# Optimization experiments

Measured on AMD Instinct MI355X. Metric: run time of the kernel, lower is better.

The kernel has to match this reference:

```python
import jax, jax.numpy as jnp
import numpy as np

B, S, D = 4, 2048, 1024  # batch, seq_len, input_dimension
KD, VD = 1024, 1024      # key_dim, value_dim


def setup_inputs() -> dict:
    key = jax.random.key(0)
    ks = jax.random.split(key, 9)
    sc_in = 1.0 / np.sqrt(D)
    sc_v = 1.0 / np.sqrt(VD)
    return {
        "x":  jax.random.normal(ks[0], (B, S, D), dtype=jnp.float32),
        "Wq": jax.random.normal(ks[1], (KD, D), dtype=jnp.float32) * sc_in,
        "bq": jax.random.normal(ks[2], (KD,), dtype=jnp.float32) * 0.01,
        "Wk": jax.random.normal(ks[3], (KD, D), dtype=jnp.float32) * sc_in,
        "bk": jax.random.normal(ks[4], (KD,), dtype=jnp.float32) * 0.01,
        "Wv": jax.random.normal(ks[5], (VD, D), dtype=jnp.float32) * sc_in,
        "bv": jax.random.normal(ks[6], (VD,), dtype=jnp.float32) * 0.01,
        "Wo": jax.random.normal(ks[7], (D, VD), dtype=jnp.float32) * sc_v,
        "bo": jax.random.normal(ks[8], (D,), dtype=jnp.float32) * 0.01,
    }


def reference(x, Wq, bq, Wk, bk, Wv, bv, Wo, bo):
    # projections (torch Linear: x @ W.T + b)
    q = jnp.einsum('bsd,kd->bsk', x, Wq) + bq   # (B,S,KD)
    k = jnp.einsum('bsd,kd->bsk', x, Wk) + bk   # (B,S,KD)
    v = jnp.einsum('bsd,vd->bsv', x, Wv) + bv   # (B,S,VD)

    scores = jnp.einsum('bqk,bsk->bqs', q, k) / jnp.sqrt(jnp.float32(KD))  # (B,S,S)

    # sign rescale: scores * sign(scores) (sign(0) mapped to 1) == |scores| with zeros kept
    sign_mask = jnp.sign(scores)
    sign_mask = sign_mask + (sign_mask == 0).astype(jnp.float32)

    # causal mask: lower-triangular (incl diag) multiplied by 1, strict upper -> -inf
    seq = scores.shape[-1]
    causal = jnp.tril(jnp.ones((seq, seq), dtype=bool))
    masked = jnp.where(causal, scores * sign_mask, -jnp.inf)

    weights = jax.nn.softmax(masked, axis=2)            # (B,S,S)
    out = jnp.einsum('bqs,bsv->bqv', weights, v)        # (B,S,VD)
    return jnp.einsum('bqv,dv->bqd', out, Wo) + bo      # (B,S,D)
```

## Files before the change

### kernel.cpp

```cpp
#include <hip/hip_runtime.h>
#include <hip/hip_bf16.h>
#include <cstdint>


#define BM 128

typedef __attribute__((ext_vector_type(8))) __bf16 bf16x8;
typedef __attribute__((ext_vector_type(4))) __bf16 bf16x4;
typedef __attribute__((ext_vector_type(4))) float floatx4;

struct Ptr3 { const float* p[3]; };

__device__ __forceinline__ void async_copy16(const __bf16* g, const __bf16* l) {
  __builtin_amdgcn_global_load_lds(
      (const __attribute__((address_space(1))) unsigned int*)(const void*)g,
      (__attribute__((address_space(3))) unsigned int*)(unsigned)(uintptr_t)(const void*)l,
      16, 0, 0);
}

__device__ __forceinline__ void gemm_core(const __bf16* __restrict__ pA,
                                          const __bf16* __restrict__ pB,
                                          int K, int kBeg, int kEnd, int mb,
                                          int nb, floatx4 (&acc)[4][4]) {
  __shared__ __align__(16) __bf16 As0[BM * 32];
  __shared__ __align__(16) __bf16 As1[BM * 32];
  __shared__ __align__(16) __bf16 Bs0[BM * 32];
  __shared__ __align__(16) __bf16 Bs1[BM * 32];

  const int t = threadIdx.x;
  const int lane = t & 63;
  const int wave = t >> 6;
  const int quad = lane >> 4;
  const int l16 = lane & 15;
  const int wm = wave >> 1;
  const int wn = wave & 1;

  const __bf16* gA = pA + (long)(mb * BM + (t >> 2)) * K + ((t & 3) * 8);
  const __bf16* gB = pB + (long)(nb * BM + (t >> 2)) * K + ((t & 3) * 8);
  const long rowHalf = (long)64 * K;
  __bf16* lA0 = &As0[t * 8];
  __bf16* lA1 = &As1[t * 8];
  __bf16* lB0 = &Bs0[t * 8];
  __bf16* lB1 = &Bs1[t * 8];

  for (int kk = kBeg; kk < kEnd; ++kk) {
    const long ko = (long)kk * 64;
    async_copy16(gA + ko, lA0);
    async_copy16(gA + ko + rowHalf, lA0 + 2048);
    async_copy16(gA + ko + 32, lA1);
    async_copy16(gA + ko + 32 + rowHalf, lA1 + 2048);
    async_copy16(gB + ko, lB0);
    async_copy16(gB + ko + rowHalf, lB0 + 2048);
    async_copy16(gB + ko + 32, lB1);
    async_copy16(gB + ko + 32 + rowHalf, lB1 + 2048);
    __syncthreads();

#pragma unroll
    for (int p = 0; p < 2; ++p) {
      const __bf16* As = p ? As1 : As0;
      const __bf16* Bs = p ? Bs1 : Bs0;
      bf16x8 af[4], bfr[4];
#pragma unroll
      for (int i = 0; i < 4; ++i) {
        af[i] = *(const bf16x8*)&As[(wm * 64 + i * 16 + l16) * 32 + quad * 8];
        bfr[i] = *(const bf16x8*)&Bs[(wn * 64 + i * 16 + l16) * 32 + quad * 8];
      }
#pragma unroll
      for (int i = 0; i < 4; ++i)
#pragma unroll
        for (int j = 0; j < 4; ++j)
          acc[i][j] = __builtin_amdgcn_mfma_f32_16x16x32_bf16(af[i], bfr[j],
                                                              acc[i][j], 0, 0, 0);
    }
    __syncthreads();
  }
}

__global__ void prep2(const float* __restrict__ Wo, Ptr3 tp,
                      const float* __restrict__ bv, const float* __restrict__ bq,
                      const float* __restrict__ bk,
                      __bf16* __restrict__ Wob, __bf16* __restrict__ Wqt,
                      __bf16* __restrict__ Wkt, __bf16* __restrict__ Wvt,
                      float* __restrict__ bvo, float* __restrict__ cscal,
                      float* __restrict__ lsum) {
  __shared__ __bf16 tile[64][66];
  __shared__ float wsum[4];
  const int bid = blockIdx.x;
  const int t = threadIdx.x;
  if (bid < 1024) {
    const long e = ((long)bid * 256 + t) * 4;
    const float4 f = *(const float4*)(Wo + e);
    bf16x4 o;
    o[0] = (__bf16)f.x; o[1] = (__bf16)f.y; o[2] = (__bf16)f.z; o[3] = (__bf16)f.w;
    *(bf16x4*)(Wob + e) = o;
  } else if (bid < 1792) {
    const int seg = (bid - 1024) >> 8;
    const int idx = (bid - 1024) & 255;
    const float* src = tp.p[seg];
    __bf16* dstw = seg == 0 ? Wqt : (seg == 1 ? Wkt : Wvt);
    const int r0 = (idx >> 4) * 64, c0 = (idx & 15) * 64;
#pragma unroll
    for (int e = 0; e < 16; ++e) {
      const int i = e * 256 + t;
      const int r = i >> 6, c = i & 63;
      tile[r][c] = (__bf16)src[(long)(r0 + r) * 1024 + (c0 + c)];
    }
    __syncthreads();
#pragma unroll
    for (int e = 0; e < 16; ++e) {
      const int i = e * 256 + t;
      const int r = i >> 6, c = i & 63;
      dstw[(long)(c0 + r) * 1024 + (r0 + c)] = tile[c][r];
    }
  } else if (bid < 2816) {
    const int d = bid - 1792;
    const float* row = Wo + (long)d * 1024;
    float s = 0.f;
    for (int v = t; v < 1024; v += 256) s += bv[v] * row[v];
#pragma unroll
    for (int off = 32; off > 0; off >>= 1) s += __shfl_down(s, off, 64);
    if ((t & 63) == 0) wsum[t >> 6] = s;
    __syncthreads();
    if (t == 0) bvo[d] = wsum[0] + wsum[1] + wsum[2] + wsum[3];
  } else if (bid == 2816) {
    float s = 0.f;
    for (int i = t; i < 1024; i += 256) s += bq[i] * bk[i];
#pragma unroll
    for (int off = 32; off > 0; off >>= 1) s += __shfl_down(s, off, 64);
    if ((t & 63) == 0) wsum[t >> 6] = s;
    __syncthreads();
    if (t == 0) *cscal = wsum[0] + wsum[1] + wsum[2] + wsum[3];
  } else {
#pragma unroll
    for (int e = 0; e < 8; ++e)
      *(float4*)(lsum + (e * 256 + t) * 4) = float4{0.f, 0.f, 0.f, 0.f};
  }
}

__global__ void __launch_bounds__(256, 3)
gemmA(const __bf16* __restrict__ Wkt, const __bf16* __restrict__ Wqt,
      const __bf16* __restrict__ Wob, const __bf16* __restrict__ Wvt,
      __bf16* __restrict__ Mt, __bf16* __restrict__ Wvo,
      const float* __restrict__ bk, const float* __restrict__ bq,
      float* __restrict__ m1f, float* __restrict__ m2f,
      const float* __restrict__ x, __bf16* __restrict__ xb) {
  const int id = blockIdx.x;
  const int t = threadIdx.x;

  if (id >= 160) {
    const long i = ((long)(id - 160) * 256 + t) * 4;
    const float4 f = *(const float4*)(x + i);
    bf16x4 o;
    o[0] = (__bf16)f.x; o[1] = (__bf16)f.y; o[2] = (__bf16)f.z; o[3] = (__bf16)f.w;
    *(bf16x4*)(xb + i) = o;
    return;
  }
  if (id >= 128) {
    const int q = (id - 128) & 15;
    const bool isM2 = (id - 128) >= 16;
    const __bf16* Wt = isM2 ? Wkt : Wqt;
    const float* bvec = isM2 ? bq : bk;
    float* dst = isM2 ? m2f : m1f;
    const int lane = t & 63, wave = t >> 6, qd = lane >> 4, l16 = lane & 15;
#pragma unroll
    for (int rr = 0; rr < 4; ++rr) {
      const int row = q * 64 + (wave * 4 + qd) * 4 + rr;
      const __bf16* wr = Wt + (long)row * 1024 + l16 * 64;
      const float* bp = bvec + l16 * 64;
      float s = 0.f;
#pragma unroll
      for (int jj = 0; jj < 8; ++jj) {
        bf16x8 wv = *(const bf16x8*)(wr + jj * 8);
#pragma unroll
        for (int e = 0; e < 8; ++e) s += (float)wv[e] * bp[jj * 8 + e];
      }
      s += __shfl_xor(s, 1, 64);
      s += __shfl_xor(s, 2, 64);
      s += __shfl_xor(s, 4, 64);
      s += __shfl_xor(s, 8, 64);
      if (l16 == 0) dst[row] = s;
    }
    return;
  }

  const __bf16 *pA, *pB;
  __bf16* dst;
  int mb, nb;
  if (id < 64) {
    mb = id >> 3; nb = id & 7;
    pA = Wkt; pB = Wqt; dst = Mt;
  } else {
    const int w = id - 64;
    mb = w >> 3; nb = w & 7;
    pA = Wob; pB = Wvt; dst = Wvo;
  }

  floatx4 acc[4][4] = {};
  gemm_core(pA, pB, 1024, 0, 16, mb, nb, acc);

  const int lane = t & 63, wave = t >> 6;
  const int rb = (wave >> 1) * 64 + (lane >> 4) * 4;
  const int cb = (wave & 1) * 64 + (lane & 15);
#pragma unroll
  for (int j4 = 0; j4 < 4; ++j4) {
    const int gc = nb * 128 + cb + j4 * 16;
#pragma unroll
    for (int i = 0; i < 4; ++i) {
      const int gr = mb * BM + rb + i * 16;
#pragma unroll
      for (int r = 0; r < 4; ++r)
        dst[(long)(gr + r) * 1024 + gc] = (__bf16)acc[i][j4][r];
    }
  }
}

__global__ void __launch_bounds__(256, 3)
gemmB1(const __bf16* __restrict__ xb, const __bf16* __restrict__ Mt,
       const float* __restrict__ m2f, __bf16* __restrict__ y2,
       const float* __restrict__ m1f, const float* __restrict__ cscal,
       float* __restrict__ uvec) {
  const int id = blockIdx.x;
  const int t = threadIdx.x;

  if (id >= 512) {
    const int k = id - 512;
    const int lane = t & 63, wave = t >> 6, qd = lane >> 4, l16 = lane & 15;
    const float c = *cscal;
#pragma unroll
    for (int rr = 0; rr < 4; ++rr) {
      const int row = k * 64 + (wave * 4 + qd) * 4 + rr;
      const __bf16* xr = xb + (long)row * 1024 + l16 * 64;
      const float* mp = m1f + l16 * 64;
      float s = 0.f;
#pragma unroll
      for (int jj = 0; jj < 8; ++jj) {
        bf16x8 xv = *(const bf16x8*)(xr + jj * 8);
#pragma unroll
        for (int e = 0; e < 8; ++e) s += (float)xv[e] * mp[jj * 8 + e];
      }
      s += __shfl_xor(s, 1, 64);
      s += __shfl_xor(s, 2, 64);
      s += __shfl_xor(s, 4, 64);
      s += __shfl_xor(s, 8, 64);
      if (l16 == 0) uvec[row] = s + c;
    }
    return;
  }

  const int xcd = id & 7;
  const int j = id >> 3;
  const int mb = xcd * 8 + (j & 7);
  const int nb = j >> 3;

  floatx4 acc[4][4] = {};
  gemm_core(xb, Mt, 1024, 0, 16, mb, nb, acc);

  const int lane = t & 63, wave = t >> 6;
  const int rb = (wave >> 1) * 64 + (lane >> 4) * 4;
  const int cb = (wave & 1) * 64 + (lane & 15);
#pragma unroll
  for (int j4 = 0; j4 < 4; ++j4) {
    const int gc = nb * 128 + cb + j4 * 16;
    const float bvv = m2f[gc];
#pragma unroll
    for (int i = 0; i < 4; ++i) {
      const int gr = mb * BM + rb + i * 16;
#pragma unroll
      for (int r = 0; r < 4; ++r)
        y2[(long)(gr + r) * 1024 + gc] = (__bf16)(acc[i][j4][r] + bvv);
    }
  }
}

__global__ void __launch_bounds__(256, 3)
gemmB2(const __bf16* __restrict__ xb, const __bf16* __restrict__ Wvo,
       const float* __restrict__ bvo, __bf16* __restrict__ Ut,
       const __bf16* __restrict__ y2, const float* __restrict__ uvec,
       __bf16* __restrict__ P, float* __restrict__ lsum,
       int S, int KD, int D) {
  const int id = blockIdx.x;
  const __bf16 *pA, *pB;
  int mb, nb, b, mode;
  if (id < 512) {
    const int xcd = id & 7;
    const int j = id >> 3;
    mb = xcd * 8 + (j & 7);
    nb = j >> 3;
    b = 0;
    mode = 0;
    pA = xb;
    pB = Wvo;
  } else {
    const int sid = id - 512;
    const int xcd = sid & 7;
    const int r = sid >> 3;
    b = r / 17;
    const int ci = r - b * 17;
    const int n1 = xcd + 1;
    mb = (ci < n1) ? xcd : (15 - xcd);
    nb = (ci < n1) ? ci : (ci - n1);
    mode = 1;
    pA = y2 + (long)b * S * KD;
    pB = xb + (long)b * S * KD;
  }

  floatx4 acc[4][4] = {};
  gemm_core(pA, pB, KD, 0, KD / 64, mb, nb, acc);

  const int t = threadIdx.x;
  const int lane = t & 63, wave = t >> 6;
  const int l16 = lane & 15;
  const int rb = (wave >> 1) * 64 + (lane >> 4) * 4;
  const int cb = (wave & 1) * 64 + l16;

  if (mode == 0) {
    const int bb = (mb * BM) / S;
    const int s0 = mb * BM - bb * S;
#pragma unroll
    for (int j4 = 0; j4 < 4; ++j4) {
      const int gc = nb * 128 + cb + j4 * 16;
      const float bv = bvo[gc];
#pragma unroll
      for (int i = 0; i < 4; ++i) {
        const int sr = s0 + rb + i * 16;
        bf16x4 o;
#pragma unroll
        for (int r = 0; r < 4; ++r) o[r] = (__bf16)(acc[i][j4][r] + bv);
        *(bf16x4*)&Ut[((long)bb * D + gc) * S + sr] = o;
      }
    }
  } else {
    __bf16* C = P + (long)b * S * S;
    float* lrow = lsum + (long)b * S;
    const float sc = 0.03125f;
#pragma unroll
    for (int i = 0; i < 4; ++i) {
#pragma unroll
      for (int r = 0; r < 4; ++r) {
        const int row = mb * BM + rb + i * 16 + r;
        const float urow = uvec[(long)b * S + row];
        float psum = 0.f;
#pragma unroll
        for (int j4 = 0; j4 < 4; ++j4) {
          const int col = nb * 128 + cb + j4 * 16;
          const float p =
              (col <= row) ? __expf(fabsf(acc[i][j4][r] + urow) * sc) : 0.f;
          psum += p;
          C[(long)row * S + col] = (__bf16)p;
        }
        psum += __shfl_xor(psum, 1, 64);
        psum += __shfl_xor(psum, 2, 64);
        psum += __shfl_xor(psum, 4, 64);
        psum += __shfl_xor(psum, 8, 64);
        if (l16 == 0) atomicAdd(&lrow[row], psum);
      }
    }
  }
}

__global__ void __launch_bounds__(256, 3)
gemm_pvo(const __bf16* __restrict__ P, const __bf16* __restrict__ Ut,
         const float* __restrict__ lsum, const float* __restrict__ bo,
         float* __restrict__ out, int S, int D) {
  const int id = blockIdx.x;
  const int xcd = id & 7;
  const int j = id >> 3;
  const int half = j >> 5;
  const int idx = j & 31;
  const int b = idx >> 3;
  const int nb = idx & 7;
  const int mb = half ? xcd : (15 - xcd);

  floatx4 acc[4][4] = {};
  gemm_core(P + (long)b * S * S, Ut + (long)b * D * S, S, 0, 2 * (mb + 1), mb,
            nb, acc);

  const int t = threadIdx.x;
  const int lane = t & 63, wave = t >> 6;
  const int rb = (wave >> 1) * 64 + (lane >> 4) * 4;
  const int cb = (wave & 1) * 64 + (lane & 15);
  const float* lrow = lsum + (long)b * S;

#pragma unroll
  for (int i = 0; i < 4; ++i) {
#pragma unroll
    for (int r = 0; r < 4; ++r) {
      const int row = mb * BM + rb + i * 16 + r;
      const float inv = 1.f / lrow[row];
#pragma unroll
      for (int j4 = 0; j4 < 4; ++j4) {
        const int col = nb * 128 + cb + j4 * 16;
        out[((long)b * S + row) * D + col] = acc[i][j4][r] * inv + bo[col];
      }
    }
  }
}

extern "C" void kernel_launch(void* const* d_in, const int* in_sizes, int n_in,
                              void* d_out, int out_size, void* d_ws, size_t ws_size,
                              hipStream_t stream) {
  const float* x = (const float*)d_in[0];
  const float* Wq = (const float*)d_in[1];
  const float* bq = (const float*)d_in[2];
  const float* Wk = (const float*)d_in[3];
  const float* bk = (const float*)d_in[4];
  const float* Wv = (const float*)d_in[5];
  const float* bv = (const float*)d_in[6];
  const float* Wo = (const float*)d_in[7];
  const float* bo = (const float*)d_in[8];
  float* out = (float*)d_out;

  constexpr int B = 4, S = 2048, D = 1024, KD = 1024;
  constexpr long MB_ = 1024 * 1024;

  char* w = (char*)d_ws;
  __bf16* xb  = (__bf16*)(w);
  __bf16* y2  = (__bf16*)(w + 16 * MB_);
  __bf16* Ut  = (__bf16*)(w + 32 * MB_);
  __bf16* P   = (__bf16*)(w + 48 * MB_);
  __bf16* Wob = (__bf16*)(w + 80 * MB_);
  __bf16* Wqt = (__bf16*)(w + 82 * MB_);
  __bf16* Wkt = (__bf16*)(w + 84 * MB_);
  __bf16* Wvt = (__bf16*)(w + 86 * MB_);
  __bf16* Mt  = (__bf16*)(w + 88 * MB_);
  __bf16* Wvo = (__bf16*)(w + 90 * MB_);
  float* lsum  = (float*)(w + 92 * MB_);
  float* uvec  = (float*)(w + 92 * MB_ + 32768);
  float* bvo   = (float*)(w + 92 * MB_ + 65536);
  float* m2f   = (float*)(w + 92 * MB_ + 69632);
  float* m1f   = (float*)(w + 92 * MB_ + 73728);
  float* cscal = (float*)(w + 92 * MB_ + 77824);

  Ptr3 tp{{Wq, Wk, Wv}};
  prep2<<<2818, 256, 0, stream>>>(Wo, tp, bv, bq, bk, Wob, Wqt, Wkt, Wvt,
                                  bvo, cscal, lsum);

  gemmA<<<8352, 256, 0, stream>>>(Wkt, Wqt, Wob, Wvt, Mt, Wvo, bk, bq,
                                  m1f, m2f, x, xb);

  gemmB1<<<640, 256, 0, stream>>>(xb, Mt, m2f, y2, m1f, cscal, uvec);

  gemmB2<<<1056, 256, 0, stream>>>(xb, Wvo, bvo, Ut, y2, uvec, P, lsum, S, KD, D);

  gemm_pvo<<<512, 256, 0, stream>>>(P, Ut, lsum, bo, out, S, D);
}
```

Before: 243.0 us.

## Triple-buffer GEMM core with async prefetch and XOR-swizzled LDS layout

Replaces the synchronous load-then-compute loop in the shared GEMM core with a three-stage ring of LDS buffers. The k-step shrinks from 64 to 32, and loads for step k+2 are issued while step k computes, using a partial vmcnt wait and a single barrier per step. An XOR swizzle on the LDS column index is meant to cut bank conflicts on the fragment reads. This hides global-load latency behind MFMA work at the cost of more LDS per block and twice as many loop iterations, and all callers are updated to the new step count.

```diff
diff --git a/kernel.cpp b/kernel.cpp
--- a/kernel.cpp
+++ b/kernel.cpp
@@ -22,10 +22,8 @@
                                           const __bf16* __restrict__ pB,
                                           int K, int kBeg, int kEnd, int mb,
                                           int nb, floatx4 (&acc)[4][4]) {
-  __shared__ __align__(16) __bf16 As0[BM * 32];
-  __shared__ __align__(16) __bf16 As1[BM * 32];
-  __shared__ __align__(16) __bf16 Bs0[BM * 32];
-  __shared__ __align__(16) __bf16 Bs1[BM * 32];
+  __shared__ __align__(16) __bf16 As[3][BM * 32];
+  __shared__ __align__(16) __bf16 Bs[3][BM * 32];
 
   const int t = threadIdx.x;
   const int lane = t & 63;
@@ -34,46 +32,52 @@
   const int l16 = lane & 15;
   const int wm = wave >> 1;
   const int wn = wave & 1;
-
-  const __bf16* gA = pA + (long)(mb * BM + (t >> 2)) * K + ((t & 3) * 8);
-  const __bf16* gB = pB + (long)(nb * BM + (t >> 2)) * K + ((t & 3) * 8);
+  const int qsw = quad ^ ((l16 >> 1) & 3);
+
+  const int srow = t >> 2;
+  const int scol = ((t & 3) ^ ((t >> 3) & 3)) * 8;
+  const __bf16* gA = pA + (long)(mb * BM + srow) * K + scol;
+  const __bf16* gB = pB + (long)(nb * BM + srow) * K + scol;
   const long rowHalf = (long)64 * K;
-  __bf16* lA0 = &As0[t * 8];
-  __bf16* lA1 = &As1[t * 8];
-  __bf16* lB0 = &Bs0[t * 8];
-  __bf16* lB1 = &Bs1[t * 8];
+
+  auto stage = [&](int kk, int buf) {
+    const long ko = (long)kk * 32;
+    __bf16* lA = &As[buf][t * 8];
+    __bf16* lB = &Bs[buf][t * 8];
+    async_copy16(gA + ko, lA);
+    async_copy16(gA + ko + rowHalf, lA + 2048);
+    async_copy16(gB + ko, lB);
+    async_copy16(gB + ko + rowHalf, lB + 2048);
+  };
+
+  stage(kBeg, 0);
+  stage(kBeg + 1 < kEnd ? kBeg + 1 : kEnd - 1, 1);
 
   for (int kk = kBeg; kk < kEnd; ++kk) {
-    const long ko = (long)kk * 64;
-    async_copy16(gA + ko, lA0);
-    async_copy16(gA + ko + rowHalf, lA0 + 2048);
-    async_copy16(gA + ko + 32, lA1);
-    async_copy16(gA + ko + 32 + rowHalf, lA1 + 2048);
-    async_copy16(gB + ko, lB0);
-    async_copy16(gB + ko + rowHalf, lB0 + 2048);
-    async_copy16(gB + ko + 32, lB1);
-    async_copy16(gB + ko + 32 + rowHalf, lB1 + 2048);
-    __syncthreads();
-
-#pragma unroll
-    for (int p = 0; p < 2; ++p) {
-      const __bf16* As = p ? As1 : As0;
-      const __bf16* Bs = p ? Bs1 : Bs0;
-      bf16x8 af[4], bfr[4];
-#pragma unroll
-      for (int i = 0; i < 4; ++i) {
-        af[i] = *(const bf16x8*)&As[(wm * 64 + i * 16 + l16) * 32 + quad * 8];
-        bfr[i] = *(const bf16x8*)&Bs[(wn * 64 + i * 16 + l16) * 32 + quad * 8];
-      }
-#pragma unroll
-      for (int i = 0; i < 4; ++i)
-#pragma unroll
-        for (int j = 0; j < 4; ++j)
-          acc[i][j] = __builtin_amdgcn_mfma_f32_16x16x32_bf16(af[i], bfr[j],
-                                                              acc[i][j], 0, 0, 0);
-    }
-    __syncthreads();
-  }
+    const int cur = (kk - kBeg) % 3;
+    asm volatile("s_waitcnt vmcnt(4)" ::: "memory");
+    __builtin_amdgcn_s_barrier();
+    __builtin_amdgcn_sched_barrier(0);
+    {
+      const int nxt = kk + 2;
+      stage(nxt < kEnd ? nxt : kEnd - 1, (cur + 2) % 3);
+    }
+    const __bf16* Asp = &As[cur][0];
+    const __bf16* Bsp = &Bs[cur][0];
+    bf16x8 af[4], bfr[4];
+#pragma unroll
+    for (int i = 0; i < 4; ++i) {
+      af[i] = *(const bf16x8*)&Asp[(wm * 64 + i * 16 + l16) * 32 + qsw * 8];
+      bfr[i] = *(const bf16x8*)&Bsp[(wn * 64 + i * 16 + l16) * 32 + qsw * 8];
+    }
+#pragma unroll
+    for (int i = 0; i < 4; ++i)
+#pragma unroll
+      for (int j = 0; j < 4; ++j)
+        acc[i][j] = __builtin_amdgcn_mfma_f32_16x16x32_bf16(af[i], bfr[j],
+                                                            acc[i][j], 0, 0, 0);
+  }
+  __syncthreads();
 }
 
 __global__ void prep2(const float* __restrict__ Wo, Ptr3 tp,
@@ -196,7 +200,7 @@
   }
 
   floatx4 acc[4][4] = {};
-  gemm_core(pA, pB, 1024, 0, 16, mb, nb, acc);
+  gemm_core(pA, pB, 1024, 0, 32, mb, nb, acc);
 
   const int lane = t & 63, wave = t >> 6;
   const int rb = (wave >> 1) * 64 + (lane >> 4) * 4;
@@ -253,7 +257,7 @@
   const int nb = j >> 3;
 
   floatx4 acc[4][4] = {};
-  gemm_core(xb, Mt, 1024, 0, 16, mb, nb, acc);
+  gemm_core(xb, Mt, 1024, 0, 32, mb, nb, acc);
 
   const int lane = t & 63, wave = t >> 6;
   const int rb = (wave >> 1) * 64 + (lane >> 4) * 4;
@@ -305,7 +309,7 @@
   }
 
   floatx4 acc[4][4] = {};
-  gemm_core(pA, pB, KD, 0, KD / 64, mb, nb, acc);
+  gemm_core(pA, pB, KD, 0, KD / 32, mb, nb, acc);
 
   const int t = threadIdx.x;
   const int lane = t & 63, wave = t >> 6;
@@ -372,7 +376,7 @@
   const int mb = half ? xcd : (15 - xcd);
 
   floatx4 acc[4][4] = {};
-  gemm_core(P + (long)b * S * S, Ut + (long)b * D * S, S, 0, 2 * (mb + 1), mb,
+  gemm_core(P + (long)b * S * S, Ut + (long)b * D * S, S, 0, 4 * (mb + 1), mb,
             nb, acc);
 
   const int t = threadIdx.x;
```

Result: faster. 237.0 us (-2.5%).
